# Performance work log

Hardware: AMD Instinct MI355X
Metric: run time of the kernel (lower is better)

The kernel has to match this reference:

```python
import jax, jax.numpy as jnp
import numpy as np

B, L, C_IN = 32, 1024, 21
D, H, DFF, MODES, LAYERS = 512, 8, 2048, 64, 2
E = D // H            # 64, matches FourierBlock weights1 [8, D//8, D//8, modes]
K_MA = 25             # moving_avg kernel
EPS = 1e-5

def _pos_encoding(n, d):
    pos = np.arange(n)[:, None].astype(np.float32)
    div = np.exp(np.arange(0, d, 2).astype(np.float32) * -(np.log(10000.0) / d))
    pe = np.zeros((n, d), np.float32)
    pe[:, 0::2] = np.sin(pos * div)
    pe[:, 1::2] = np.cos(pos * div)
    return jnp.asarray(pe)

PE = _pos_encoding(L, D)

def _moving_avg(x, k):
    # series_decomp: replicate-pad (k-1)//2 on both ends, then mean window k
    pad = (k - 1) // 2
    xp = jnp.pad(x, ((0, 0), (pad, pad), (0, 0)), mode='edge')
    return jax.lax.reduce_window(xp, 0.0, jax.lax.add, (1, k, 1), (1, 1, 1), 'VALID') / k

def _layernorm(x, g, b):
    mu = x.mean(-1, keepdims=True)
    var = ((x - mu) ** 2).mean(-1, keepdims=True)
    return (x - mu) * jax.lax.rsqrt(var + EPS) * g + b

def _fourier_block(q, w_cplx):
    # q: [B,L,H,E] -> [B,H,E,L]; keep only lowest MODES frequencies,
    # complex per-mode channel mixing, then inverse rFFT.
    x = q.transpose(0, 2, 3, 1)
    x_ft = jnp.fft.rfft(x, axis=-1)                          # [B,H,E,L//2+1] complex
    out_m = jnp.einsum('bhem,heom->bhom', x_ft[..., :MODES], w_cplx)
    out_ft = jnp.zeros(x_ft.shape[:3] + (L // 2 + 1,), jnp.complex64)
    out_ft = out_ft.at[..., :MODES].set(out_m)
    return jnp.fft.irfft(out_ft, n=L, axis=-1)               # [B,H,E,L] real

def _forward(x_enc, conv_w, wq, bq, wo, bo, fw_re, fw_im, conv1_w, conv2_w,
             enc_g, enc_b, ff_w, ff_b, ffn_g, ffn_b, reg_w, reg_b):
    # DataEmbedding_onlypos: circular Conv1d(k=3, no bias) + sinusoidal PE (dropout=0)
    xt = x_enc.transpose(0, 2, 1)                            # [B,C,L]
    xp = jnp.pad(xt, ((0, 0), (0, 0), (1, 1)), mode='wrap')
    emb = jax.lax.conv_general_dilated(xp, conv_w, (1,), 'VALID',
                                       dimension_numbers=('NCH', 'OIH', 'NCH'))
    x = emb.transpose(0, 2, 1) + PE                          # [B,L,D]
    for l in range(LAYERS):
        # AutoCorrelationLayer: only the query projection feeds FourierBlock
        q = (jnp.einsum('bld,kd->blk', x, wq[l]) + bq[l]).reshape(B, L, H, E)
        new_x = _fourier_block(q, fw_re[l] + 1j * fw_im[l])  # [B,H,E,L]
        # torch .view(B, L, -1) on contiguous [B,H,E,L] = raw reshape
        new_x = new_x.reshape(B, L, H * E)
        new_x = jnp.einsum('bld,kd->blk', new_x, wo[l]) + bo[l]
        x = x + new_x
        x = x - _moving_avg(x, K_MA)                         # decomp1 -> residual part
        y = jax.nn.gelu(jnp.einsum('bld,fd->blf', x, conv1_w[l]), approximate=False)
        y = jnp.einsum('blf,df->bld', y, conv2_w[l])
        xy = x + y
        x = xy - _moving_avg(xy, K_MA)                       # decomp2 -> residual part
    # my_Layernorm: LN then subtract per-sequence mean
    x = _layernorm(x, enc_g, enc_b)
    x = x - x.mean(axis=1, keepdims=True)
    x = _layernorm(jnp.einsum('bld,kd->blk', x, ff_w) + ff_b, ffn_g, ffn_b)
    flat = x.reshape(B, L * D)
    return flat @ reg_w.T + reg_b                            # [B,1]

def setup_inputs():
    key = jax.random.key(0)
    ks = jax.random.split(key, 12)
    r = lambda k, shp, s=0.02: jax.random.normal(k, shp, jnp.float32) * s
    scale = 1.0 / (D * D)
    return {
        'x_enc': jax.random.normal(ks[0], (B, L, C_IN), jnp.float32),
        'conv_w': r(ks[1], (D, C_IN, 3), 0.05),
        'wq': r(ks[2], (LAYERS, D, D)),
        'bq': jnp.zeros((LAYERS, D), jnp.float32),
        'wo': r(ks[3], (LAYERS, D, D)),
        'bo': jnp.zeros((LAYERS, D), jnp.float32),
        'fw_re': jax.random.uniform(ks[4], (LAYERS, H, E, E, MODES), jnp.float32) * scale,
        'fw_im': jax.random.uniform(ks[5], (LAYERS, H, E, E, MODES), jnp.float32) * scale,
        'conv1_w': r(ks[6], (LAYERS, DFF, D)),
        'conv2_w': r(ks[7], (LAYERS, D, DFF)),
        'enc_g': jnp.ones((D,), jnp.float32),
        'enc_b': jnp.zeros((D,), jnp.float32),
        'ff_w': r(ks[8], (D, D)),
        'ff_b': jnp.zeros((D,), jnp.float32),
        'ffn_g': jnp.ones((D,), jnp.float32),
        'ffn_b': jnp.zeros((D,), jnp.float32),
        'reg_w': r(ks[9], (1, D * L)),
        'reg_b': jnp.zeros((1,), jnp.float32),
    }

def reference(x_enc, conv_w, wq, bq, wo, bo, fw_re, fw_im, conv1_w, conv2_w,
              enc_g, enc_b, ff_w, ff_b, ffn_g, ffn_b, reg_w, reg_b):
    return _forward(x_enc, conv_w, wq, bq, wo, bo, fw_re, fw_im, conv1_w, conv2_w,
                    enc_g, enc_b, ff_w, ff_b, ffn_g, ffn_b, reg_w, reg_b)
```

## Files before the change

kernel.cpp:

```cpp
#include <hip/hip_runtime.h>
#include <math.h>

static constexpr int B_   = 32;
static constexpr int L_   = 1024;
static constexpr int CIN_ = 21;
static constexpr int D_   = 512;
static constexpr int H_   = 8;
static constexpr int E_   = 64;
static constexpr int DFF_ = 2048;
static constexpr int M_   = 64;

typedef unsigned short u16;
typedef __attribute__((ext_vector_type(8))) short bf16x8;
typedef __attribute__((ext_vector_type(4))) float f32x4;
typedef __attribute__((ext_vector_type(4))) unsigned short u16x4;

static __device__ __forceinline__ u16 f2b(float f) {
    unsigned u = __float_as_uint(f);
    unsigned r = (u + 0x7fffu + ((u >> 16) & 1u)) >> 16;
    return (u16)r;
}
static __device__ __forceinline__ float b2f(u16 x) {
    return __uint_as_float((unsigned)x << 16);
}

static __device__ __forceinline__ void gload16(const u16* g, u16* l) {
    unsigned long long ga = (unsigned long long)g;
    unsigned la = (unsigned)(unsigned long long)l;
    __builtin_amdgcn_global_load_lds(
        (const __attribute__((address_space(1))) void*)ga,
        (__attribute__((address_space(3))) void*)(unsigned long long)la,
        16, 0, 0);
}

__global__ void k_tables(u16* trig, u16* tcat, float* pe) {
    int idx = blockIdx.x * 256 + threadIdx.x;
    if (idx < 131072) {
        int l = idx & 1023, mc = idx >> 10;
        int m = mc & 63;
        float th = (float)((m * l) & 1023) * 0.006135923151542565f;
        float v = (mc < 64) ? cosf(th) : (-sinf(th));
        trig[idx] = f2b(v);
    }
    if (idx < 131072) {
        int k = idx & 127, l = idx >> 7;
        int m = k & 63;
        float th = (float)((m * l) & 1023) * 0.006135923151542565f;
        float v;
        if (k < 64) v = (m == 0) ? 1.0f : (2.0f * cosf(th));
        else        v = (m == 0) ? 0.0f : (-2.0f * sinf(th));
        tcat[idx] = f2b(v * (1.0f / 1024.0f));
    }
    if (idx < 524288) {
        int d = idx & 511, l = idx >> 9;
        int i2 = d >> 1;
        float div = expf(-(float)(2 * i2) * 0.017988946039015984f);
        float arg = (float)l * div;
        pe[idx] = (d & 1) ? cosf(arg) : sinf(arg);
    }
}

__global__ void k_cast(const float* __restrict__ in, u16* __restrict__ out, int n4) {
    int i = blockIdx.x * 256 + threadIdx.x;
    if (i < n4) {
        float4 v = ((const float4*)in)[i];
        u16x4 o = { f2b(v.x), f2b(v.y), f2b(v.z), f2b(v.w) };
        ((u16x4*)out)[i] = o;
    }
}

__global__ void k_wtrans(const float* __restrict__ re, const float* __restrict__ im,
                         u16* __restrict__ outre, u16* __restrict__ outim) {
    __shared__ float t[64][65];
    const float* src = blockIdx.z ? im : re;
    u16* dst = blockIdx.z ? outim : outre;
    int h = blockIdx.y, eo0 = blockIdx.x * 64;
    int j = threadIdx.x & 63, i0 = threadIdx.x >> 6;
    for (int i = i0; i < 64; i += 4)
        t[i][j] = src[(size_t)h * 262144 + (size_t)(eo0 + i) * 64 + j];
    __syncthreads();
    for (int i = i0; i < 64; i += 4)
        dst[(size_t)h * 262144 + (size_t)i * 4096 + eo0 + j] = f2b(t[j][i]);
}

__global__ __launch_bounds__(512) void k_embed(
        const float* __restrict__ xe, const float* __restrict__ cw,
        const float* __restrict__ pe, float* __restrict__ x32,
        u16* __restrict__ x16) {
    __shared__ float strip[34][21];
    int b = blockIdx.y, l0 = blockIdx.x * 32;
    int d = threadIdx.x;
    for (int i = d; i < 34 * 21; i += 512) {
        int r = i / 21, c = i - r * 21;
        int ls = (l0 + r - 1 + 1024) & 1023;
        strip[r][c] = xe[((size_t)b * 1024 + ls) * 21 + c];
    }
    __syncthreads();
    float w[3][21];
    #pragma unroll
    for (int k = 0; k < 3; ++k)
        #pragma unroll
        for (int c = 0; c < 21; ++c)
            w[k][c] = cw[(size_t)d * 63 + c * 3 + k];
    float a0[21], a1[21];
    #pragma unroll
    for (int c = 0; c < 21; ++c) { a0[c] = strip[0][c]; a1[c] = strip[1][c]; }
    for (int li = 0; li < 32; ++li) {
        float acc = 0.f;
        #pragma unroll
        for (int c = 0; c < 21; ++c) {
            float a2 = strip[li + 2][c];
            acc += w[0][c] * a0[c] + w[1][c] * a1[c] + w[2][c] * a2;
            a0[c] = a1[c]; a1[c] = a2;
        }
        int l = l0 + li;
        float v = acc + pe[(size_t)l * 512 + d];
        size_t o = ((size_t)b * 1024 + l) * 512 + d;
        x32[o] = v;
        x16[o] = f2b(v);
    }
}

template<bool BIAS, bool BIASR, bool GELU, bool ADD, bool WF32, bool WBF16,
         bool DFTZ = false>
__global__ __launch_bounds__(256, 3) void k_mfma(
        const u16* __restrict__ A, const u16* __restrict__ W,
        const float* __restrict__ bias, const float* addp,
        float* C32, u16* C16,
        int K, int lda, int ldw, int ldc, long strideA, long strideC) {
    __shared__ __align__(16) u16 As[128 * 32];
    __shared__ __align__(16) u16 Bs[128 * 32];
    const int tid  = threadIdx.x;
    const int lane = tid & 63, wid = tid >> 6;
    int m0, n0;
    size_t cbase;
    if constexpr (DFTZ) {
        int z  = blockIdx.z;
        int ks = z >> 5;
        m0 = 0;
        n0 = blockIdx.x * 128;
        A += (size_t)ks * 256;
        W += (size_t)(z & 31) * 1024 + (size_t)ks * 256;
        cbase = (size_t)z * 65536;
    } else {
        m0 = blockIdx.y * 128;
        n0 = blockIdx.x * 128;
        A += (size_t)blockIdx.z * strideA;
        cbase = (size_t)blockIdx.z * strideC;
    }

    const int srow = lane >> 2, scol = (lane & 3) * 8;
    const u16* ga0 = A + (size_t)(m0 + wid * 32 + srow) * lda + scol;
    const u16* ga1 = ga0 + (size_t)16 * lda;
    const u16* gb0 = W + (size_t)(n0 + wid * 32 + srow) * ldw + scol;
    const u16* gb1 = gb0 + (size_t)16 * ldw;
    u16* la0 = &As[wid * 32 * 32];
    u16* la1 = la0 + 16 * 32;
    u16* lb0 = &Bs[wid * 32 * 32];
    u16* lb1 = lb0 + 16 * 32;

    const int wr = wid >> 1, wc = wid & 1;
    const int fr = lane & 15, fg = lane >> 4;

    f32x4 acc[4][4];
    #pragma unroll
    for (int i = 0; i < 4; ++i)
        #pragma unroll
        for (int j = 0; j < 4; ++j)
            acc[i][j] = f32x4{0.f, 0.f, 0.f, 0.f};

    for (int k0 = 0; k0 < K; k0 += 32) {
        __syncthreads();
        gload16(ga0 + k0, la0);
        gload16(ga1 + k0, la1);
        gload16(gb0 + k0, lb0);
        gload16(gb1 + k0, lb1);
        __syncthreads();
        bf16x8 af[4], bfr[4];
        #pragma unroll
        for (int i = 0; i < 4; ++i) {
            af[i]  = *(const bf16x8*)&As[(wr * 64 + i * 16 + fr) * 32 + fg * 8];
            bfr[i] = *(const bf16x8*)&Bs[(wc * 64 + i * 16 + fr) * 32 + fg * 8];
        }
        #pragma unroll
        for (int i = 0; i < 4; ++i)
            #pragma unroll
            for (int j = 0; j < 4; ++j)
                acc[i][j] = __builtin_amdgcn_mfma_f32_16x16x32_bf16(
                    af[i], bfr[j], acc[i][j], 0, 0, 0);
    }

    #pragma unroll
    for (int i = 0; i < 4; ++i) {
        #pragma unroll
        for (int j = 0; j < 4; ++j) {
            #pragma unroll
            for (int r = 0; r < 4; ++r) {
                int row = m0 + wr * 64 + i * 16 + fg * 4 + r;
                int col = n0 + wc * 64 + j * 16 + fr;
                float v = acc[i][j][r];
                if (BIAS)  v += bias[col];
                if (BIASR) v += bias[row];
                if (GELU) v = 0.5f * v * (1.f + erff(v * 0.70710678118f));
                size_t o = cbase + (size_t)row * ldc + col;
                if (ADD)  v += addp[o];
                if (WF32) C32[o] = v;
                if (WBF16) C16[o] = f2b(v);
            }
        }
    }
}

__global__ void k_modemix(const float* __restrict__ ftT,
                          const u16* __restrict__ wtre, const u16* __restrict__ wtim,
                          u16* __restrict__ acat) {
    __shared__ float wr_s[64][64];
    __shared__ float wi_s[64][64];
    __shared__ float fr_s[32][64];
    __shared__ float fi_s[32][64];
    int h = blockIdx.x >> 6, m = blockIdx.x & 63;
    int tid = threadIdx.x;
    const u16* wr_p = wtre + ((size_t)(h * 64 + m)) * 4096;
    const u16* wi_p = wtim + ((size_t)(h * 64 + m)) * 4096;
    for (int i = tid; i < 4096; i += 256) {
        wr_s[i >> 6][i & 63] = b2f(wr_p[i]);
        wi_s[i >> 6][i & 63] = b2f(wi_p[i]);
    }
    const size_t KS = (size_t)32 * 65536;
    for (int i = tid; i < 2048; i += 256) {
        int b = i >> 6, e = i & 63;
        size_t f0 = (size_t)b * 65536 + (size_t)m * 512 + h * 64 + e;
        size_t f1 = f0 + (size_t)64 * 512;
        fr_s[b][e] = ftT[f0] + ftT[f0 + KS] + ftT[f0 + 2 * KS] + ftT[f0 + 3 * KS];
        fi_s[b][e] = ftT[f1] + ftT[f1 + KS] + ftT[f1 + 2 * KS] + ftT[f1 + 3 * KS];
    }
    __syncthreads();
    int o = tid & 63, bg = tid >> 6;
    for (int bb = bg; bb < 32; bb += 4) {
        float accr = 0.f, acci = 0.f;
        #pragma unroll 8
        for (int e = 0; e < 64; ++e) {
            float wr = wr_s[e][o], wi = wi_s[e][o];
            float fr = fr_s[bb][e], fi = fi_s[bb][e];
            accr += fr * wr - fi * wi;
            acci += fr * wi + fi * wr;
        }
        size_t base = (((size_t)(bb * 8 + h)) * 64 + o) * 128;
        acat[base + m]      = f2b(accr);
        acat[base + 64 + m] = f2b(acci);
    }
}

__global__ void k_madiff(const float* __restrict__ in, float* __restrict__ out,
                         u16* __restrict__ out16) {
    int b = blockIdx.x, dg = blockIdx.y, ls = blockIdx.z;
    int d = dg * 256 + threadIdx.x;
    const float* base = in + (size_t)b * 524288 + d;
    int l0 = ls * 64;
    float sum = 0.f;
    #pragma unroll
    for (int k = -12; k <= 12; ++k) {
        int ll = l0 + k;
        ll = ll < 0 ? 0 : (ll > 1023 ? 1023 : ll);
        sum += base[(size_t)ll * 512];
    }
    for (int li = 0; li < 64; ++li) {
        int l = l0 + li;
        float x = base[(size_t)l * 512];
        float v = x - sum * (1.f / 25.f);
        size_t o = (size_t)b * 524288 + (size_t)l * 512 + d;
        out[o] = v;
        out16[o] = f2b(v);
        int lp = l + 13; lp = lp > 1023 ? 1023 : lp;
        int lm = l - 12; lm = lm < 0 ? 0 : lm;
        sum += base[(size_t)lp * 512] - base[(size_t)lm * 512];
    }
}

__global__ void k_layernorm(const float* __restrict__ in, const float* __restrict__ g,
                            const float* __restrict__ bta, float* __restrict__ out) {
    int row = blockIdx.x;
    int tid = threadIdx.x;
    const float* r = in + (size_t)row * 512;
    float v0 = r[tid], v1 = r[tid + 256];
    float s = v0 + v1, s2 = v0 * v0 + v1 * v1;
    #pragma unroll
    for (int off = 32; off; off >>= 1) {
        s  += __shfl_down(s, off);
        s2 += __shfl_down(s2, off);
    }
    __shared__ float ws[4], ws2[4];
    if ((tid & 63) == 0) { ws[tid >> 6] = s; ws2[tid >> 6] = s2; }
    __syncthreads();
    if (tid == 0) {
        ws[0]  = ws[0] + ws[1] + ws[2] + ws[3];
        ws2[0] = ws2[0] + ws2[1] + ws2[2] + ws2[3];
    }
    __syncthreads();
    float mu = ws[0] * (1.f / 512.f);
    float var = ws2[0] * (1.f / 512.f) - mu * mu;
    float rs = rsqrtf(var + 1e-5f);
    float* o = out + (size_t)row * 512;
    o[tid]       = (v0 - mu) * rs * g[tid]       + bta[tid];
    o[tid + 256] = (v1 - mu) * rs * g[tid + 256] + bta[tid + 256];
}

__global__ void k_lnreg(const float* __restrict__ in, const float* __restrict__ g,
                        const float* __restrict__ bta, const float* __restrict__ rw,
                        float* __restrict__ partial) {
    int row = blockIdx.x;
    int tid = threadIdx.x;
    const float* r = in + (size_t)row * 512;
    float v0 = r[tid], v1 = r[tid + 256];
    float s = v0 + v1, s2 = v0 * v0 + v1 * v1;
    #pragma unroll
    for (int off = 32; off; off >>= 1) {
        s  += __shfl_down(s, off);
        s2 += __shfl_down(s2, off);
    }
    __shared__ float ws[4], ws2[4];
    if ((tid & 63) == 0) { ws[tid >> 6] = s; ws2[tid >> 6] = s2; }
    __syncthreads();
    if (tid == 0) {
        ws[0]  = ws[0] + ws[1] + ws[2] + ws[3];
        ws2[0] = ws2[0] + ws2[1] + ws2[2] + ws2[3];
    }
    __syncthreads();
    float mu = ws[0] * (1.f / 512.f);
    float var = ws2[0] * (1.f / 512.f) - mu * mu;
    float rs = rsqrtf(var + 1e-5f);
    const float* wrow = rw + (size_t)(row & 1023) * 512;
    float y0 = (v0 - mu) * rs * g[tid]       + bta[tid];
    float y1 = (v1 - mu) * rs * g[tid + 256] + bta[tid + 256];
    float p = y0 * wrow[tid] + y1 * wrow[tid + 256];
    #pragma unroll
    for (int off = 32; off; off >>= 1) p += __shfl_down(p, off);
    __shared__ float wp[4];
    if ((tid & 63) == 0) wp[tid >> 6] = p;
    __syncthreads();
    if (tid == 0) partial[row] = wp[0] + wp[1] + wp[2] + wp[3];
}

__global__ void k_regf2(const float* __restrict__ partial, const float* __restrict__ rb,
                        float* __restrict__ out) {
    int b = blockIdx.x;
    int tid = threadIdx.x;
    const float* p = partial + (size_t)b * 1024;
    float s = p[tid] + p[tid + 256] + p[tid + 512] + p[tid + 768];
    #pragma unroll
    for (int off = 32; off; off >>= 1) s += __shfl_down(s, off);
    __shared__ float ws[4];
    if ((tid & 63) == 0) ws[tid >> 6] = s;
    __syncthreads();
    if (tid == 0) out[b] = ws[0] + ws[1] + ws[2] + ws[3] + rb[0];
}

__global__ __launch_bounds__(512) void k_colmean1(const float* __restrict__ in,
                                                  float* __restrict__ part) {
    int b = blockIdx.x, seg = blockIdx.y;
    int d = threadIdx.x;
    const float* p = in + ((size_t)b * 1024 + seg * 128) * 512 + d;
    float s = 0.f;
    for (int l = 0; l < 128; ++l) s += p[(size_t)l * 512];
    part[((size_t)b * 8 + seg) * 512 + d] = s;
}

__global__ void k_colmean2(const float* __restrict__ part, float* __restrict__ mean) {
    int i = blockIdx.x * 256 + threadIdx.x;
    int b = i >> 9, d = i & 511;
    float s = 0.f;
    #pragma unroll
    for (int seg = 0; seg < 8; ++seg) s += part[((size_t)b * 8 + seg) * 512 + d];
    mean[i] = s * (1.f / 1024.f);
}

__global__ void k_subcol(float* __restrict__ x, const float* __restrict__ mean,
                         u16* __restrict__ x16) {
    int idx = blockIdx.x * 256 + threadIdx.x;
    int d = idx & 511;
    int b = idx >> 19;
    float v = x[idx] - mean[b * 512 + d];
    x[idx] = v;
    x16[idx] = f2b(v);
}

extern "C" void kernel_launch(void* const* d_in, const int* in_sizes, int n_in,
                              void* d_out, int out_size, void* d_ws, size_t ws_size,
                              hipStream_t stream) {
    const float* x_enc  = (const float*)d_in[0];
    const float* conv_w = (const float*)d_in[1];
    const float* wq     = (const float*)d_in[2];
    const float* bq     = (const float*)d_in[3];
    const float* wo     = (const float*)d_in[4];
    const float* bo     = (const float*)d_in[5];
    const float* fw_re  = (const float*)d_in[6];
    const float* fw_im  = (const float*)d_in[7];
    const float* c1w    = (const float*)d_in[8];
    const float* c2w    = (const float*)d_in[9];
    const float* enc_g  = (const float*)d_in[10];
    const float* enc_b  = (const float*)d_in[11];
    const float* ff_w   = (const float*)d_in[12];
    const float* ff_b   = (const float*)d_in[13];
    const float* ffn_g  = (const float*)d_in[14];
    const float* ffn_b  = (const float*)d_in[15];
    const float* reg_w  = (const float*)d_in[16];
    const float* reg_b  = (const float*)d_in[17];
    float* out = (float*)d_out;

    char* wsb = (char*)d_ws;
    float* F0    = (float*)(wsb);
    float* F1    = (float*)(wsb + 67108864);
    u16*   A16   = (u16*)  (wsb + 134217728);
    u16*   U16   = (u16*)  (wsb + 167772160);
    u16*   AC16  = (u16*)  (wsb + 201326592);
    float* FTT   = (float*)(wsb + 205520896);
    float* PE    = (float*)(wsb + 213909504);
    u16*   TRIG  = (u16*)  (wsb + 216006656);
    u16*   TCAT  = (u16*)  (wsb + 216268800);
    u16*   WQ16  = (u16*)  (wsb + 216530944);
    u16*   WO16  = (u16*)  (wsb + 217579520);
    u16*   C1W16 = (u16*)  (wsb + 218628096);
    u16*   C2W16 = (u16*)  (wsb + 222822400);
    u16*   FFW16 = (u16*)  (wsb + 227016704);
    float* CMEAN = (float*)(wsb + 227540992);
    const size_t need_bytes = 227606528;
    if (ws_size < need_bytes) return;

    u16* WTRE16 = (u16*)FTT;
    u16* WTIM16 = WTRE16 + 2097152;

    const int BLD = B_ * L_ * D_;
    dim3 blk(256);

    k_tables<<<2048, blk, 0, stream>>>(TRIG, TCAT, PE);
    k_cast<<<512,  blk, 0, stream>>>(wq,   WQ16,  524288 / 4);
    k_cast<<<512,  blk, 0, stream>>>(wo,   WO16,  524288 / 4);
    k_cast<<<2048, blk, 0, stream>>>(c1w,  C1W16, 2097152 / 4);
    k_cast<<<2048, blk, 0, stream>>>(c2w,  C2W16, 2097152 / 4);
    k_cast<<<256,  blk, 0, stream>>>(ff_w, FFW16, 262144 / 4);
    k_embed<<<dim3(32, 32), 512, 0, stream>>>(x_enc, conv_w, PE, F0, A16);

    float* cur = F0;
    float* alt = F1;
    const dim3 g_big(4, 256);

    for (int l = 0; l < 2; ++l) {
        const float* bq_l = bq + l * 512;
        const float* bo_l = bo + l * 512;
        const u16* wo16_l = WO16 + (size_t)l * 262144;
        const u16* c1_l   = C1W16 + (size_t)l * DFF_ * D_;
        const u16* c2_l   = C2W16 + (size_t)l * D_ * DFF_;
        const float* fwre_l = fw_re + (size_t)l * H_ * E_ * E_ * M_;
        const float* fwim_l = fw_im + (size_t)l * H_ * E_ * E_ * M_;

        k_wtrans<<<dim3(64, 8, 2), blk, 0, stream>>>(fwre_l, fwim_l, WTRE16, WTIM16);
        k_mfma<false, true, false, false, false, true><<<dim3(256, 4), blk, 0, stream>>>(
            WQ16 + (size_t)l * 262144, A16, bq_l, nullptr, nullptr, U16,
            512, 512, 512, 32768, 0, 0);
        float* ftt4 = alt;
        k_mfma<false, false, false, false, true, false, true>
            <<<dim3(4, 1, 128), blk, 0, stream>>>(
            TRIG, U16, nullptr, nullptr, ftt4, nullptr,
            256, 1024, 32768, 512, 0, 0);
        k_modemix<<<512, blk, 0, stream>>>(ftt4, WTRE16, WTIM16, AC16);
        k_mfma<false, false, false, false, false, true><<<dim3(8, 128), blk, 0, stream>>>(
            AC16, TCAT, nullptr, nullptr, nullptr, U16, 128, 128, 128, 1024, 0, 0);
        k_mfma<true, false, false, true, true, false><<<g_big, blk, 0, stream>>>(
            U16, wo16_l, bo_l, cur, cur, nullptr, 512, 512, 512, 512, 0, 0);
        k_madiff<<<dim3(32, 2, 16), blk, 0, stream>>>(cur, alt, A16);
        { float* t = cur; cur = alt; alt = t; }
        u16* y16 = (u16*)alt;
        for (int c = 0; c < 2; ++c) {
            const size_t aoff = (size_t)c * 16384 * 512;
            k_mfma<false, false, true, false, false, true><<<dim3(16, 128), blk, 0, stream>>>(
                A16 + aoff, c1_l, nullptr, nullptr, nullptr, y16,
                512, 512, 512, 2048, 0, 0);
            k_mfma<false, false, false, true, true, false><<<dim3(4, 128), blk, 0, stream>>>(
                y16, c2_l, nullptr, cur + aoff, cur + aoff, nullptr,
                2048, 2048, 2048, 512, 0, 0);
        }
        k_madiff<<<dim3(32, 2, 16), blk, 0, stream>>>(cur, alt, A16);
        { float* t = cur; cur = alt; alt = t; }
    }

    k_layernorm<<<32768, blk, 0, stream>>>(cur, enc_g, enc_b, alt);
    k_colmean1<<<dim3(B_, 8), 512, 0, stream>>>(alt, FTT);
    k_colmean2<<<64, blk, 0, stream>>>(FTT, CMEAN);
    k_subcol<<<BLD / 256, blk, 0, stream>>>(alt, CMEAN, A16);
    k_mfma<true, false, false, false, true, false><<<g_big, blk, 0, stream>>>(
        A16, FFW16, ff_b, nullptr, cur, nullptr, 512, 512, 512, 512, 0, 0);
    k_lnreg<<<32768, blk, 0, stream>>>(cur, ffn_g, ffn_b, reg_w, FTT);
    k_regf2<<<32, blk, 0, stream>>>(FTT, reg_b, out);
}
```

Measured before the change: 1.194 ms.

## Double GEMM K-tile to 64, vectorize moving-average kernel, refine embed grid

```diff
diff --git a/kernel.cpp b/kernel.cpp
--- a/kernel.cpp
+++ b/kernel.cpp
@@ -87,11 +87,11 @@
         const float* __restrict__ xe, const float* __restrict__ cw,
         const float* __restrict__ pe, float* __restrict__ x32,
         u16* __restrict__ x16) {
-    __shared__ float strip[34][21];
-    int b = blockIdx.y, l0 = blockIdx.x * 32;
+    __shared__ float strip[18][21];
+    int b = blockIdx.y, l0 = blockIdx.x * 16;
     int d = threadIdx.x;
-    for (int i = d; i < 34 * 21; i += 512) {
-        int r = i / 21, c = i - r * 21;
+    if (d < 18 * 21) {
+        int r = d / 21, c = d - r * 21;
         int ls = (l0 + r - 1 + 1024) & 1023;
         strip[r][c] = xe[((size_t)b * 1024 + ls) * 21 + c];
     }
@@ -105,7 +105,7 @@
     float a0[21], a1[21];
     #pragma unroll
     for (int c = 0; c < 21; ++c) { a0[c] = strip[0][c]; a1[c] = strip[1][c]; }
-    for (int li = 0; li < 32; ++li) {
+    for (int li = 0; li < 16; ++li) {
         float acc = 0.f;
         #pragma unroll
         for (int c = 0; c < 21; ++c) {
@@ -128,8 +128,8 @@
         const float* __restrict__ bias, const float* addp,
         float* C32, u16* C16,
         int K, int lda, int ldw, int ldc, long strideA, long strideC) {
-    __shared__ __align__(16) u16 As[128 * 32];
-    __shared__ __align__(16) u16 Bs[128 * 32];
+    __shared__ __align__(16) u16 As[128 * 64];
+    __shared__ __align__(16) u16 Bs[128 * 64];
     const int tid  = threadIdx.x;
     const int lane = tid & 63, wid = tid >> 6;
     int m0, n0;
@@ -149,15 +149,9 @@
         cbase = (size_t)blockIdx.z * strideC;
     }
 
-    const int srow = lane >> 2, scol = (lane & 3) * 8;
-    const u16* ga0 = A + (size_t)(m0 + wid * 32 + srow) * lda + scol;
-    const u16* ga1 = ga0 + (size_t)16 * lda;
-    const u16* gb0 = W + (size_t)(n0 + wid * 32 + srow) * ldw + scol;
-    const u16* gb1 = gb0 + (size_t)16 * ldw;
-    u16* la0 = &As[wid * 32 * 32];
-    u16* la1 = la0 + 16 * 32;
-    u16* lb0 = &Bs[wid * 32 * 32];
-    u16* lb1 = lb0 + 16 * 32;
+    const int srow = lane >> 3, scol = (lane & 7) * 8;
+    const u16* gaP = A + (size_t)(m0 + wid * 32 + srow) * lda + scol;
+    const u16* gbP = W + (size_t)(n0 + wid * 32 + srow) * ldw + scol;
 
     const int wr = wid >> 1, wc = wid & 1;
     const int fr = lane & 15, fg = lane >> 4;
@@ -169,25 +163,29 @@
         for (int j = 0; j < 4; ++j)
             acc[i][j] = f32x4{0.f, 0.f, 0.f, 0.f};
 
-    for (int k0 = 0; k0 < K; k0 += 32) {
+    for (int k0 = 0; k0 < K; k0 += 64) {
         __syncthreads();
-        gload16(ga0 + k0, la0);
-        gload16(ga1 + k0, la1);
-        gload16(gb0 + k0, lb0);
-        gload16(gb1 + k0, lb1);
+        #pragma unroll
+        for (int i = 0; i < 4; ++i) {
+            gload16(gaP + (size_t)(8 * i) * lda + k0, &As[(wid * 32 + 8 * i) * 64]);
+            gload16(gbP + (size_t)(8 * i) * ldw + k0, &Bs[(wid * 32 + 8 * i) * 64]);
+        }
         __syncthreads();
-        bf16x8 af[4], bfr[4];
-        #pragma unroll
-        for (int i = 0; i < 4; ++i) {
-            af[i]  = *(const bf16x8*)&As[(wr * 64 + i * 16 + fr) * 32 + fg * 8];
-            bfr[i] = *(const bf16x8*)&Bs[(wc * 64 + i * 16 + fr) * 32 + fg * 8];
-        }
-        #pragma unroll
-        for (int i = 0; i < 4; ++i)
+        #pragma unroll
+        for (int ks = 0; ks < 2; ++ks) {
+            bf16x8 af[4], bfr[4];
             #pragma unroll
-            for (int j = 0; j < 4; ++j)
-                acc[i][j] = __builtin_amdgcn_mfma_f32_16x16x32_bf16(
-                    af[i], bfr[j], acc[i][j], 0, 0, 0);
+            for (int i = 0; i < 4; ++i) {
+                af[i]  = *(const bf16x8*)&As[(wr * 64 + i * 16 + fr) * 64 + ks * 32 + fg * 8];
+                bfr[i] = *(const bf16x8*)&Bs[(wc * 64 + i * 16 + fr) * 64 + ks * 32 + fg * 8];
+            }
+            #pragma unroll
+            for (int i = 0; i < 4; ++i)
+                #pragma unroll
+                for (int j = 0; j < 4; ++j)
+                    acc[i][j] = __builtin_amdgcn_mfma_f32_16x16x32_bf16(
+                        af[i], bfr[j], acc[i][j], 0, 0, 0);
+        }
     }
 
     #pragma unroll
@@ -253,27 +251,32 @@
 
 __global__ void k_madiff(const float* __restrict__ in, float* __restrict__ out,
                          u16* __restrict__ out16) {
-    int b = blockIdx.x, dg = blockIdx.y, ls = blockIdx.z;
-    int d = dg * 256 + threadIdx.x;
-    const float* base = in + (size_t)b * 524288 + d;
+    int b = blockIdx.x, ls = blockIdx.y;
+    int d2 = threadIdx.x;
+    const float2* base = (const float2*)(in + (size_t)b * 524288) + d2;
     int l0 = ls * 64;
-    float sum = 0.f;
+    float sx = 0.f, sy = 0.f;
     #pragma unroll
     for (int k = -12; k <= 12; ++k) {
         int ll = l0 + k;
         ll = ll < 0 ? 0 : (ll > 1023 ? 1023 : ll);
-        sum += base[(size_t)ll * 512];
+        float2 v = base[(size_t)ll * 256];
+        sx += v.x; sy += v.y;
     }
     for (int li = 0; li < 64; ++li) {
         int l = l0 + li;
-        float x = base[(size_t)l * 512];
-        float v = x - sum * (1.f / 25.f);
-        size_t o = (size_t)b * 524288 + (size_t)l * 512 + d;
-        out[o] = v;
-        out16[o] = f2b(v);
+        float2 x = base[(size_t)l * 256];
+        float vx = x.x - sx * (1.f / 25.f);
+        float vy = x.y - sy * (1.f / 25.f);
+        size_t o = (size_t)b * 262144 + (size_t)l * 256 + d2;
+        ((float2*)out)[o] = float2{vx, vy};
+        unsigned pk = (unsigned)f2b(vx) | ((unsigned)f2b(vy) << 16);
+        ((unsigned*)out16)[o] = pk;
         int lp = l + 13; lp = lp > 1023 ? 1023 : lp;
         int lm = l - 12; lm = lm < 0 ? 0 : lm;
-        sum += base[(size_t)lp * 512] - base[(size_t)lm * 512];
+        float2 a = base[(size_t)lp * 256];
+        float2 s = base[(size_t)lm * 256];
+        sx += a.x - s.x; sy += a.y - s.y;
     }
 }
 
@@ -438,7 +441,7 @@
     k_cast<<<2048, blk, 0, stream>>>(c1w,  C1W16, 2097152 / 4);
     k_cast<<<2048, blk, 0, stream>>>(c2w,  C2W16, 2097152 / 4);
     k_cast<<<256,  blk, 0, stream>>>(ff_w, FFW16, 262144 / 4);
-    k_embed<<<dim3(32, 32), 512, 0, stream>>>(x_enc, conv_w, PE, F0, A16);
+    k_embed<<<dim3(64, 32), 512, 0, stream>>>(x_enc, conv_w, PE, F0, A16);
 
     float* cur = F0;
     float* alt = F1;
@@ -467,7 +470,7 @@
             AC16, TCAT, nullptr, nullptr, nullptr, U16, 128, 128, 128, 1024, 0, 0);
         k_mfma<true, false, false, true, true, false><<<g_big, blk, 0, stream>>>(
             U16, wo16_l, bo_l, cur, cur, nullptr, 512, 512, 512, 512, 0, 0);
-        k_madiff<<<dim3(32, 2, 16), blk, 0, stream>>>(cur, alt, A16);
+        k_madiff<<<dim3(32, 16), blk, 0, stream>>>(cur, alt, A16);
         { float* t = cur; cur = alt; alt = t; }
         u16* y16 = (u16*)alt;
         for (int c = 0; c < 2; ++c) {
@@ -479,7 +482,7 @@
                 y16, c2_l, nullptr, cur + aoff, cur + aoff, nullptr,
                 2048, 2048, 2048, 512, 0, 0);
         }
-        k_madiff<<<dim3(32, 2, 16), blk, 0, stream>>>(cur, alt, A16);
+        k_madiff<<<dim3(32, 16), blk, 0, stream>>>(cur, alt, A16);
         { float* t = cur; cur = alt; alt = t; }
     }
 
```

Result: slower. 1.246 ms (+4.3%).
